# Kernel tuning notes

Measured on AMD Instinct MI355X. Metric: run time of the kernel, lower is better.

## Reference

```python
import jax, jax.numpy as jnp
import numpy as np

B, T, U = 8, 256, 64
ENC_DIM, DEC_DIM, JOINT_DIM, VOCAB = 512, 512, 640, 1024


def setup_inputs() -> dict:
    key = jax.random.key(0)
    k1, k2, k3, k4, k5 = jax.random.split(key, 5)
    s_enc = 1.0 / np.sqrt(ENC_DIM)
    s_dec = 1.0 / np.sqrt(DEC_DIM)
    s_joint = 1.0 / np.sqrt(JOINT_DIM)
    return {
        "enc_out": jax.random.normal(k1, (B, T, ENC_DIM), dtype=jnp.float32),
        "pred_out": jax.random.normal(k2, (B, U, DEC_DIM), dtype=jnp.float32),
        # nn.Linear weights stored as [out, in], applied as x @ W.T
        "W_enc": jax.random.uniform(k3, (JOINT_DIM, ENC_DIM), jnp.float32, -s_enc, s_enc),
        "W_pred": jax.random.uniform(k4, (JOINT_DIM, DEC_DIM), jnp.float32, -s_dec, s_dec),
        "W_out": jax.random.uniform(k5, (VOCAB, JOINT_DIM), jnp.float32, -s_joint, s_joint),
    }


def reference(enc_out, pred_out, W_enc, W_pred, W_out):
    # project: [B,T,J] and [B,U,J]
    enc_p = jnp.einsum("bte,je->btj", enc_out, W_enc)
    pred_p = jnp.einsum("bud,jd->buj", pred_out, W_pred)
    # broadcast add -> [B,T,U,J], SiLU, then output GEMM -> [B,T,U,V]
    joint = enc_p[:, :, None, :] + pred_p[:, None, :, :]
    joint = joint * jax.nn.sigmoid(joint)  # SiLU
    out = jnp.einsum("btuj,vj->btuv", joint, W_out)
    return out
```

## Files before the change

kernel.cpp:

```cpp
#include <hip/hip_runtime.h>

typedef unsigned short u16;
typedef __attribute__((ext_vector_type(8))) short short8;
typedef __attribute__((ext_vector_type(8))) unsigned short ushort8v;
typedef __attribute__((ext_vector_type(4))) float f32x4;

#define B_ 8
#define T_ 256
#define U_ 64
#define E_ 512
#define J_ 640
#define V_ 1024
#define NT 20

__device__ __forceinline__ u16 f2bf(float f) {
  unsigned int u = __float_as_uint(f);
  u += 0x7fffu + ((u >> 16) & 1u);
  return (u16)(u >> 16);
}

__device__ __forceinline__ void gload16(const void* g, void* l) {
  __builtin_amdgcn_global_load_lds((const __attribute__((address_space(1))) void*)g,
                                   (__attribute__((address_space(3))) void*)l,
                                   16, 0, 0);
}

__global__ __launch_bounds__(256) void cast5_k(const float4* __restrict__ s0,
                                               const float4* __restrict__ s1,
                                               const float4* __restrict__ s2,
                                               const float4* __restrict__ s3,
                                               const float4* __restrict__ s4,
                                               ushort4* __restrict__ dst) {
  int i = blockIdx.x * 256 + threadIdx.x;
  const int st = gridDim.x * 256;
  for (; i < 655360; i += st) {
    const float4* s; int off;
    if (i < 262144)      { s = s0; off = 0; }
    else if (i < 327680) { s = s1; off = 262144; }
    else if (i < 409600) { s = s2; off = 327680; }
    else if (i < 491520) { s = s3; off = 409600; }
    else                 { s = s4; off = 491520; }
    float4 v = s[i - off];
    ushort4 o;
    o.x = f2bf(v.x); o.y = f2bf(v.y); o.z = f2bf(v.z); o.w = f2bf(v.w);
    dst[i] = o;
  }
}

__global__ __launch_bounds__(256) void proj_k(const u16* __restrict__ X,
                                              const u16* __restrict__ W,
                                              float* __restrict__ C) {
  __shared__ __align__(16) u16 As[128 * 32];
  __shared__ __align__(16) u16 Bs[128 * 32];
  const int tid = threadIdx.x;
  const int w = tid >> 6, lane = tid & 63;
  const int wr = w >> 1, wc = w & 1;
  const int m0 = blockIdx.x * 128, n0 = blockIdx.y * 128;
  const int lr = lane & 15, lk = lane >> 4;
  const int r4 = tid >> 2, kq = tid & 3;

  f32x4 acc[4][4] = {};

  for (int ks = 0; ks < E_ / 32; ++ks) {
    const int k0 = ks * 32;
    gload16(X + (size_t)(m0 + r4) * E_ + k0 + kq * 8, (char*)As + w * 1024);
    gload16(X + (size_t)(m0 + 64 + r4) * E_ + k0 + kq * 8, (char*)As + 4096 + w * 1024);
    gload16(W + (size_t)(n0 + r4) * E_ + k0 + kq * 8, (char*)Bs + w * 1024);
    gload16(W + (size_t)(n0 + 64 + r4) * E_ + k0 + kq * 8, (char*)Bs + 4096 + w * 1024);
    __syncthreads();
    short8 a[4], bb[4];
#pragma unroll
    for (int m = 0; m < 4; ++m)
      a[m] = *(const short8*)&As[(wr * 64 + m * 16 + lr) * 32 + lk * 8];
#pragma unroll
    for (int n = 0; n < 4; ++n)
      bb[n] = *(const short8*)&Bs[(wc * 64 + n * 16 + lr) * 32 + lk * 8];
#pragma unroll
    for (int m = 0; m < 4; ++m)
#pragma unroll
      for (int n = 0; n < 4; ++n)
        acc[m][n] = __builtin_amdgcn_mfma_f32_16x16x32_bf16(a[m], bb[n], acc[m][n], 0, 0, 0);
    __syncthreads();
  }

#pragma unroll
  for (int m = 0; m < 4; ++m) {
    const int row = m0 + wr * 64 + m * 16 + lk * 4;
#pragma unroll
    for (int n = 0; n < 4; ++n) {
      const int col = n0 + wc * 64 + n * 16 + lr;
#pragma unroll
      for (int i = 0; i < 4; ++i)
        C[(size_t)(row + i) * J_ + col] = acc[m][n][i];
    }
  }
}

__global__ __launch_bounds__(256) void pack_k(const u16* __restrict__ Wo,
                                              u16* __restrict__ pk) {
  const int u = blockIdx.x * 256 + threadIdx.x;
  const int l = u & 63;
  int r = u >> 6;
  const int nq = r & 3;  r >>= 2;
  const int ks = r % 20;
  const int vt = r / 20;
  const int v = vt * 64 + nq * 16 + (l & 15);
  const int k = ks * 32 + (l >> 4) * 8;
  *(short8*)(pk + (size_t)u * 8) = *(const short8*)(Wo + (size_t)v * J_ + k);
}

__global__ __launch_bounds__(1024, 1) void fused3_k(const float* __restrict__ ep,
                                                    const float* __restrict__ pp,
                                                    const u16* __restrict__ pk,
                                                    float* __restrict__ out) {
  __shared__ __align__(16) u16 Alds[64 * 640];
  const int tid = threadIdx.x;
  const int w = tid >> 6, lane = tid & 63;
  const int lr = lane & 15, lk = lane >> 4;
  const int bt = blockIdx.x;
  const int b = bt >> 8;
  const size_t m0 = (size_t)bt * 64;

  const u16* bp = pk + (size_t)w * 40960 + lane * 8;

  short8 BE[4], BO[4], a[4];

#define BL(bF, ks)                                                             \
  do {                                                                         \
    _Pragma("unroll")                                                          \
    for (int nq = 0; nq < 4; ++nq)                                             \
      bF[nq] = *(const short8*)(bp + (ks) * 2048 + nq * 512);                  \
  } while (0)

  BL(BE, 0);

  const float* eprow = ep + (size_t)bt * J_;
  const float* pbase = pp + (size_t)b * 64 * J_;
#pragma unroll
  for (int it = 0; it < 5; ++it) {
    const int unit = tid + it * 1024;
    const int row = unit / 80;
    const int c = unit - row * 80;
    union { float4 v[2]; float f[8]; } Ee, Pp;
    Ee.v[0] = *(const float4*)(eprow + c * 8);
    Ee.v[1] = *(const float4*)(eprow + c * 8 + 4);
    Pp.v[0] = *(const float4*)(pbase + (size_t)row * J_ + c * 8);
    Pp.v[1] = *(const float4*)(pbase + (size_t)row * J_ + c * 8 + 4);
    union { ushort8v v; u16 s[8]; } R;
#pragma unroll
    for (int j = 0; j < 8; ++j) {
      float x = Ee.f[j] + Pp.f[j];
      R.s[j] = f2bf(x * __builtin_amdgcn_rcpf(1.0f + __expf(-x)));
    }
    *(ushort8v*)&Alds[row * 640 + ((c ^ (row & 7)) << 3)] = R.v;
  }
  __syncthreads();

  const int rx = lr & 7;

#define AR(ks)                                                                 \
  do {                                                                         \
    _Pragma("unroll")                                                          \
    for (int mq = 0; mq < 4; ++mq)                                             \
      a[mq] = *(const short8*)&Alds[(mq * 16 + lr) * 640 +                     \
                                    ((((ks) * 4 + lk) ^ rx) << 3)];            \
  } while (0)

#define MM(bF)                                                                 \
  do {                                                                         \
    __builtin_amdgcn_s_setprio(1);                                             \
    _Pragma("unroll")                                                          \
    for (int mq = 0; mq < 4; ++mq)                                             \
      _Pragma("unroll")                                                        \
      for (int nq = 0; nq < 4; ++nq)                                           \
        acc[mq][nq] = __builtin_amdgcn_mfma_f32_16x16x32_bf16(bF[nq], a[mq],   \
                                                              acc[mq][nq], 0, 0, 0); \
    __builtin_amdgcn_s_setprio(0);                                             \
  } while (0)

  f32x4 acc[4][4] = {};

#pragma unroll 1
  for (int ks = 0; ks < NT; ks += 2) {
    AR(ks);
    BL(BO, ks + 1);
    MM(BE);
    __builtin_amdgcn_sched_barrier(0);
    AR(ks + 1);
    if (ks + 2 < NT) BL(BE, ks + 2);
    MM(BO);
    __builtin_amdgcn_sched_barrier(0);
  }

#pragma unroll
  for (int mq = 0; mq < 4; ++mq) {
    const size_t row = m0 + mq * 16 + lr;
#pragma unroll
    for (int nq = 0; nq < 4; ++nq) {
      const int col = w * 64 + nq * 16 + lk * 4;
      *(float4*)&out[row * V_ + col] = *(float4*)&acc[mq][nq];
    }
  }
#undef AR
#undef BL
#undef MM
}

extern "C" void kernel_launch(void* const* d_in, const int* in_sizes, int n_in,
                              void* d_out, int out_size, void* d_ws, size_t ws_size,
                              hipStream_t stream) {
  const float* enc = (const float*)d_in[0];
  const float* pred = (const float*)d_in[1];
  const float* We = (const float*)d_in[2];
  const float* Wp = (const float*)d_in[3];
  const float* Wo = (const float*)d_in[4];
  float* out = (float*)d_out;

  char* ws = (char*)d_ws;
  u16* enc_bf = (u16*)ws;
  u16* pred_bf = (u16*)(ws + 2097152);
  u16* We_bf = (u16*)(ws + 2621440);
  u16* Wp_bf = (u16*)(ws + 3276800);
  u16* Wo_bf = (u16*)(ws + 3932160);
  float* ep = (float*)(ws + 5242880);
  float* pp = (float*)(ws + 10485760);
  u16* Wo_pk = (u16*)(ws + 11796480);

  cast5_k<<<2048, 256, 0, stream>>>((const float4*)enc, (const float4*)pred,
                                    (const float4*)We, (const float4*)Wp,
                                    (const float4*)Wo, (ushort4*)ws);

  proj_k<<<dim3(16, 5), 256, 0, stream>>>(enc_bf, We_bf, ep);
  proj_k<<<dim3(4, 5), 256, 0, stream>>>(pred_bf, Wp_bf, pp);
  pack_k<<<320, 256, 0, stream>>>(Wo_bf, Wo_pk);

  fused3_k<<<2048, 1024, 0, stream>>>(ep, pp, Wo_pk, out);
}
```

Measured before the change: 249.7 us.

## Halve waves per block, each wave computes two vocab tiles with overlapped stores

The fused joint kernel now runs 512 threads (8 waves) per block instead of 1024, and each wave computes two 64-column vocab tiles in sequence using two accumulator sets. Stores of the first tile's results are interleaved into the MFMA loop of the second tile, hiding output write latency behind compute. B-fragment prefetch crosses from the first tile into the second. This halves the A-staging work per wave ratio but doubles accumulator registers (64 extra VGPRs), which risks spills or lower occupancy.

```diff
diff --git a/kernel.cpp b/kernel.cpp
--- a/kernel.cpp
+++ b/kernel.cpp
@@ -109,10 +109,10 @@
   *(short8*)(pk + (size_t)u * 8) = *(const short8*)(Wo + (size_t)v * J_ + k);
 }
 
-__global__ __launch_bounds__(1024, 1) void fused3_k(const float* __restrict__ ep,
-                                                    const float* __restrict__ pp,
-                                                    const u16* __restrict__ pk,
-                                                    float* __restrict__ out) {
+__global__ __launch_bounds__(512, 1) void fused8_k(const float* __restrict__ ep,
+                                                   const float* __restrict__ pp,
+                                                   const u16* __restrict__ pk,
+                                                   float* __restrict__ out) {
   __shared__ __align__(16) u16 Alds[64 * 640];
   const int tid = threadIdx.x;
   const int w = tid >> 6, lane = tid & 63;
@@ -120,25 +120,27 @@
   const int bt = blockIdx.x;
   const int b = bt >> 8;
   const size_t m0 = (size_t)bt * 64;
-
-  const u16* bp = pk + (size_t)w * 40960 + lane * 8;
+  const int rx = lr & 7;
+
+  const u16* bp0 = pk + (size_t)(2 * w) * 40960 + lane * 8;
+  const u16* bp1 = bp0 + 40960;
 
   short8 BE[4], BO[4], a[4];
 
-#define BL(bF, ks)                                                             \
+#define BL(bF, bp, ks)                                                         \
   do {                                                                         \
     _Pragma("unroll")                                                          \
     for (int nq = 0; nq < 4; ++nq)                                             \
-      bF[nq] = *(const short8*)(bp + (ks) * 2048 + nq * 512);                  \
-  } while (0)
-
-  BL(BE, 0);
+      bF[nq] = *(const short8*)((bp) + (ks) * 2048 + nq * 512);                \
+  } while (0)
+
+  BL(BE, bp0, 0);
 
   const float* eprow = ep + (size_t)bt * J_;
   const float* pbase = pp + (size_t)b * 64 * J_;
 #pragma unroll
-  for (int it = 0; it < 5; ++it) {
-    const int unit = tid + it * 1024;
+  for (int it = 0; it < 10; ++it) {
+    const int unit = tid + it * 512;
     const int row = unit / 80;
     const int c = unit - row * 80;
     union { float4 v[2]; float f[8]; } Ee, Pp;
@@ -156,8 +158,6 @@
   }
   __syncthreads();
 
-  const int rx = lr & 7;
-
 #define AR(ks)                                                                 \
   do {                                                                         \
     _Pragma("unroll")                                                          \
@@ -166,44 +166,60 @@
                                     ((((ks) * 4 + lk) ^ rx) << 3)];            \
   } while (0)
 
-#define MM(bF)                                                                 \
+#define MM(bF, ACC)                                                            \
   do {                                                                         \
     __builtin_amdgcn_s_setprio(1);                                             \
     _Pragma("unroll")                                                          \
     for (int mq = 0; mq < 4; ++mq)                                             \
       _Pragma("unroll")                                                        \
       for (int nq = 0; nq < 4; ++nq)                                           \
-        acc[mq][nq] = __builtin_amdgcn_mfma_f32_16x16x32_bf16(bF[nq], a[mq],   \
-                                                              acc[mq][nq], 0, 0, 0); \
+        ACC[mq][nq] = __builtin_amdgcn_mfma_f32_16x16x32_bf16(bF[nq], a[mq],   \
+                                                              ACC[mq][nq], 0, 0, 0); \
     __builtin_amdgcn_s_setprio(0);                                             \
   } while (0)
 
-  f32x4 acc[4][4] = {};
-
-#pragma unroll 1
-  for (int ks = 0; ks < NT; ks += 2) {
-    AR(ks);
-    BL(BO, ks + 1);
-    MM(BE);
-    __builtin_amdgcn_sched_barrier(0);
-    AR(ks + 1);
-    if (ks + 2 < NT) BL(BE, ks + 2);
-    MM(BO);
-    __builtin_amdgcn_sched_barrier(0);
-  }
-
-#pragma unroll
-  for (int mq = 0; mq < 4; ++mq) {
-    const size_t row = m0 + mq * 16 + lr;
-#pragma unroll
-    for (int nq = 0; nq < 4; ++nq) {
-      const int col = w * 64 + nq * 16 + lk * 4;
-      *(float4*)&out[row * V_ + col] = *(float4*)&acc[mq][nq];
-    }
-  }
+#define ST1(ACC, idx, vtc)                                                     \
+  do {                                                                         \
+    const int mq_ = (idx) >> 2, nq_ = (idx) & 3;                               \
+    *(float4*)&out[(m0 + mq_ * 16 + lr) * V_ + (vtc) * 64 + nq_ * 16 + lk * 4] = \
+        *(float4*)&ACC[mq_][nq_];                                              \
+  } while (0)
+
+  f32x4 accA[4][4] = {}, accB[4][4] = {};
+
+#pragma unroll
+  for (int it = 0; it < 10; ++it) {
+    BL(BO, bp0, 2 * it + 1);
+    AR(2 * it);
+    MM(BE, accA);
+    __builtin_amdgcn_sched_barrier(0);
+    if (it < 9) BL(BE, bp0, 2 * it + 2);
+    else        BL(BE, bp1, 0);
+    AR(2 * it + 1);
+    MM(BO, accA);
+    __builtin_amdgcn_sched_barrier(0);
+  }
+
+#pragma unroll
+  for (int it = 0; it < 10; ++it) {
+    BL(BO, bp1, 2 * it + 1);
+    AR(2 * it);
+    MM(BE, accB);
+    if (2 * it < 16) ST1(accA, 2 * it, 2 * w);
+    __builtin_amdgcn_sched_barrier(0);
+    if (it < 9) BL(BE, bp1, 2 * it + 2);
+    AR(2 * it + 1);
+    MM(BO, accB);
+    if (2 * it + 1 < 16) ST1(accA, 2 * it + 1, 2 * w);
+    __builtin_amdgcn_sched_barrier(0);
+  }
+
+#pragma unroll
+  for (int idx = 0; idx < 16; ++idx) ST1(accB, idx, 2 * w + 1);
+#undef BL
 #undef AR
-#undef BL
 #undef MM
+#undef ST1
 }
 
 extern "C" void kernel_launch(void* const* d_in, const int* in_sizes, int n_in,
@@ -234,5 +250,5 @@
   proj_k<<<dim3(4, 5), 256, 0, stream>>>(pred_bf, Wp_bf, pp);
   pack_k<<<320, 256, 0, stream>>>(Wo_bf, Wo_pk);
 
-  fused3_k<<<2048, 1024, 0, stream>>>(ep, pp, Wo_pk, out);
-}
+  fused8_k<<<2048, 512, 0, stream>>>(ep, pp, Wo_pk, out);
+}
```

Result: no change. 253.3 us (+1.5%).
